# Performance work log

Measured on AMD Instinct MI355X. Metric: run time of the kernel, lower is better.

The kernel has to match this reference:

```python
import jax, jax.numpy as jnp
import numpy as np

B, T, K, V = 64, 256, 32, 32  # batch, trace_len, net_k, vocab_len


def setup_inputs() -> dict:
    key = jax.random.key(0)
    k1, k2, k3 = jax.random.split(key, 3)
    x = jax.random.uniform(k1, (B, T, V), dtype=jnp.float32)
    w_right = jax.random.normal(k2, (K, K + 1), dtype=jnp.float32)
    w_op = jax.random.normal(k3, (K, 5 + V), dtype=jnp.float32)
    return {"x": x, "w_right": w_right, "w_op": w_op}


def _myrelu(z):
    # CenteredLayer: x<0 -> 0.01*x ; x>1 -> 0.01*x + 0.99 ; else identity
    return jnp.where(z < 0, 0.01 * z, jnp.where(z > 1, 0.01 * z + 0.99, z))


def reference(x, w_right, w_op):
    Bs, Ts, Vs = x.shape
    Ks = w_right.shape[0]
    # cal_softmax()
    sm_op = jax.nn.softmax(w_op, axis=1)
    op_w = sm_op[:, :5].T          # (5, K) operator selection weights
    atom_w = sm_op[:, 5:].T        # (V, K)
    right_w = jax.nn.softmax(w_right, axis=1)[:, :-1].T  # (K, K)

    # atom_x is loop-invariant (x and atom_w do not change across iterations)
    atom_x = jnp.einsum('btv,vk->btk', x, atom_w)  # (B, T, K)
    zcol = jnp.zeros((Bs, Ts, 1), x.dtype)   # last_x (always zeros)
    zrow = jnp.zeros((Bs, 1, Ks), x.dtype)   # end_x  (always zeros)

    def step(all_x, _):
        left = jnp.concatenate([all_x[:, :, 1:], zcol], axis=2)          # shift node dim
        right = jnp.einsum('btk,kj->btj', all_x, right_w)                # right-child mix
        nxt = all_x[:, 1:]                                               # (B, T-1, K)
        X_left = jnp.concatenate(
            [jnp.concatenate([nxt[:, :, 1:], zcol[:, 1:]], axis=2), zrow], axis=1)
        nxt_full = jnp.concatenate([nxt, zrow], axis=1)                  # (B, T, K)
        until = right + _myrelu(left + nxt_full - 1.0)
        new = _myrelu(atom_x
                      + (1.0 - left) * op_w[1]            # not
                      + X_left * op_w[3]                  # next (X)
                      + (left + right - 1.0) * op_w[2]    # and
                      + until * op_w[4])                  # until
        return new, None

    init = jnp.zeros((Bs, Ts, Ks), x.dtype)
    all_x, _ = jax.lax.scan(step, init, None, length=Ts + Ks)
    return jax.nn.sigmoid((all_x - 0.5) * 5.0)
```

## Files before the change

### kernel.cpp

```cpp
#include <hip/hip_runtime.h>
#include <math.h>

#define BB 64
#define TT 256
#define KK 32
#define VV 32
#define CH 64
#define PH 32
#define ROWS (CH + PH)
#define NPHASE ((TT + KK) / PH)
#define BPB (TT / CH)
#define NW (ROWS / 16)

#define RW_OFF    0
#define WOP_OFF   1024
#define ATOM_OFF  2240
#define STATE_OFF (ATOM_OFF + BB*TT*KK)

typedef __attribute__((ext_vector_type(8))) short short8;
typedef __attribute__((ext_vector_type(4))) float floatx4;

__device__ __forceinline__ float myrelu(float z) {
    float c = fminf(fmaxf(z, 0.f), 1.f);
    return fmaf(0.01f, z, 0.99f * c);
}
__device__ __forceinline__ ushort f2bf(float f) {
    union { float f; unsigned int u; } v; v.f = f;
    unsigned int r = v.u + 0x7fffu + ((v.u >> 16) & 1u);
    return (ushort)(r >> 16);
}

__global__ void prep_kernel(const float* __restrict__ w_right,
                            const float* __restrict__ w_op,
                            float* __restrict__ ws) {
    int tid = threadIdx.x;
    float* rw  = ws + RW_OFF;
    float* wop = ws + WOP_OFF;
    if (tid < KK) {
        float v[37];
        float m = -1e30f;
        #pragma unroll
        for (int i = 0; i < 37; ++i) { v[i] = w_op[tid * 37 + i]; m = fmaxf(m, v[i]); }
        float s = 0.f;
        #pragma unroll
        for (int i = 0; i < 37; ++i) { v[i] = expf(v[i] - m); s += v[i]; }
        float inv = 1.f / s;
        #pragma unroll
        for (int i = 0; i < 37; ++i) wop[i * KK + tid] = v[i] * inv;
    } else if (tid < 2 * KK) {
        int r = tid - KK;
        float v[KK + 1];
        float m = -1e30f;
        #pragma unroll
        for (int i = 0; i <= KK; ++i) { v[i] = w_right[r * (KK + 1) + i]; m = fmaxf(m, v[i]); }
        float s = 0.f;
        #pragma unroll
        for (int i = 0; i <= KK; ++i) { v[i] = expf(v[i] - m); s += v[i]; }
        float inv = 1.f / s;
        #pragma unroll
        for (int c = 0; c < KK; ++c) rw[c * KK + r] = v[c] * inv;
    }
}

__global__ void atomx_kernel(const float* __restrict__ x, float* __restrict__ ws) {
    const float* aw = ws + WOP_OFF + 5 * KK;
    float* atom = ws + ATOM_OFF;
    int tid = threadIdx.x;
    int k  = tid & (KK - 1);
    int bt = blockIdx.x * 8 + (tid >> 5);
    const float* xrow = x + bt * VV;
    float acc = 0.f;
    #pragma unroll
    for (int v = 0; v < VV; ++v) acc = fmaf(xrow[v], aw[v * KK + k], acc);
    atom[bt * KK + k] = acc;
}

__global__ __launch_bounds__(384, 1)
void phase_kernel(float* __restrict__ ws, float* __restrict__ out,
                  int first, int last) {
    __shared__ float brow[2][NW + 1][36];

    const float* rw   = ws + RW_OFF;
    const float* wop  = ws + WOP_OFF;
    const float* atom = ws + ATOM_OFF;
    float*      state = ws + STATE_OFF;

    int tid  = threadIdx.x;
    int lane = tid & 63;
    int rt   = tid >> 6;
    int lr   = lane & 15;
    int hi   = lane >> 4;
    int b  = blockIdx.x / BPB;
    int c  = blockIdx.x % BPB;
    int lo = c * CH;
    int t0 = lo + rt * 16 + lr;
    bool active = (lo + rt * 16) < TT;

    for (int i = tid; i < 2 * (NW + 1) * 36; i += 384)
        (&brow[0][0][0])[i] = 0.f;

    float* gs = state + (size_t)b * TT * KK;

    float y[8];
    #pragma unroll
    for (int q = 0; q < 8; ++q) y[q] = 0.f;
    if (active && !first) {
        float4 v0 = *reinterpret_cast<const float4*>(&gs[t0 * KK + hi * 8]);
        float4 v1 = *reinterpret_cast<const float4*>(&gs[t0 * KK + hi * 8 + 4]);
        y[0] = v0.x; y[1] = v0.y; y[2] = v0.z; y[3] = v0.w;
        y[4] = v1.x; y[5] = v1.y; y[6] = v1.z; y[7] = v1.w;
    }

    float c0[8], d1[8], w2v[8], w3v[8], w4v[8];
    {
        float4 av0 = make_float4(0, 0, 0, 0), av1 = make_float4(0, 0, 0, 0);
        if (active) {
            av0 = *reinterpret_cast<const float4*>(&atom[((size_t)b * TT + t0) * KK + hi * 8]);
            av1 = *reinterpret_cast<const float4*>(&atom[((size_t)b * TT + t0) * KK + hi * 8 + 4]);
        }
        float av[8] = {av0.x, av0.y, av0.z, av0.w, av1.x, av1.y, av1.z, av1.w};
        #pragma unroll
        for (int q = 0; q < 8; ++q) {
            int j = hi * 8 + q;
            float w1 = wop[1 * KK + j];
            float w2 = wop[2 * KK + j];
            c0[q]  = av[q] + w1 - w2;
            d1[q]  = w2 - w1;
            w2v[q] = w2;
            w3v[q] = wop[3 * KK + j];
            w4v[q] = wop[4 * KK + j];
        }
    }

    short8 af0, af1;
    {
        int col0 = ((lr >> 2) << 3) | (lr & 3);
        #pragma unroll
        for (int q = 0; q < 8; ++q) {
            af0[q] = (short)f2bf(rw[(hi * 8 + q) * KK + col0]);
            af1[q] = (short)f2bf(rw[(hi * 8 + q) * KK + col0 + 4]);
        }
    }

    __syncthreads();
    if (active && lr == 0) {
        *reinterpret_cast<float4*>(&brow[0][rt][hi * 8])     = make_float4(y[0], y[1], y[2], y[3]);
        *reinterpret_cast<float4*>(&brow[0][rt][hi * 8 + 4]) = make_float4(y[4], y[5], y[6], y[7]);
    }
    __syncthreads();

    for (int s = 0; s < PH; ++s) {
        int cur = s & 1;
        if (active) {
            unsigned bw0, bw1, bw2, bw3;
            asm("v_cvt_pk_bf16_f32 %0, %1, %2" : "=v"(bw0) : "v"(y[0]), "v"(y[1]));
            asm("v_cvt_pk_bf16_f32 %0, %1, %2" : "=v"(bw1) : "v"(y[2]), "v"(y[3]));
            asm("v_cvt_pk_bf16_f32 %0, %1, %2" : "=v"(bw2) : "v"(y[4]), "v"(y[5]));
            asm("v_cvt_pk_bf16_f32 %0, %1, %2" : "=v"(bw3) : "v"(y[6]), "v"(y[7]));
            union { unsigned u[4]; short8 v; } bu;
            bu.u[0] = bw0; bu.u[1] = bw1; bu.u[2] = bw2; bu.u[3] = bw3;
            floatx4 acc0 = __builtin_amdgcn_mfma_f32_16x16x32_bf16(
                af0, bu.v, (floatx4){0.f, 0.f, 0.f, 0.f}, 0, 0, 0);
            floatx4 acc1 = __builtin_amdgcn_mfma_f32_16x16x32_bf16(
                af1, bu.v, (floatx4){0.f, 0.f, 0.f, 0.f}, 0, 0, 0);

            float nx[8];
            #pragma unroll
            for (int q = 0; q < 8; ++q) nx[q] = __shfl(y[q], lane + 1, 64);
            float lb = __shfl(y[0], lane + 16, 64);
            float xb = __shfl(y[0], lane + 17, 64);
            if (lr == 15) {
                float4 n0 = *reinterpret_cast<const float4*>(&brow[cur][rt + 1][hi * 8]);
                float4 n1 = *reinterpret_cast<const float4*>(&brow[cur][rt + 1][hi * 8 + 4]);
                nx[0] = n0.x; nx[1] = n0.y; nx[2] = n0.z; nx[3] = n0.w;
                nx[4] = n1.x; nx[5] = n1.y; nx[6] = n1.z; nx[7] = n1.w;
                xb = brow[cur][rt + 1][hi * 8 + 8];
            } else if (hi == 3) {
                xb = 0.f;
            }
            if (hi == 3) lb = 0.f;

            float le[8], xl[8];
            #pragma unroll
            for (int q = 0; q < 7; ++q) { le[q] = y[q + 1]; xl[q] = nx[q + 1]; }
            le[7] = lb; xl[7] = xb;

            #pragma unroll
            for (int q = 0; q < 8; ++q) {
                float rtv = (q < 4) ? acc0[q] : acc1[q - 4];
                float a = le[q] + nx[q] - 1.f;
                float until = rtv + myrelu(a);
                float z = fmaf(until, w4v[q],
                          fmaf(xl[q], w3v[q],
                          fmaf(rtv, w2v[q],
                          fmaf(le[q], d1[q], c0[q]))));
                y[q] = myrelu(z);
            }
        }
        if (active && lr == 0) {
            *reinterpret_cast<float4*>(&brow[cur ^ 1][rt][hi * 8])     = make_float4(y[0], y[1], y[2], y[3]);
            *reinterpret_cast<float4*>(&brow[cur ^ 1][rt][hi * 8 + 4]) = make_float4(y[4], y[5], y[6], y[7]);
        }
        __syncthreads();
    }

    if (rt < CH / 16) {
        if (last) {
            float* op = out + ((size_t)b * TT + t0) * KK + hi * 8;
            float o[8];
            #pragma unroll
            for (int q = 0; q < 8; ++q)
                o[q] = 1.f / (1.f + __expf(-5.f * (y[q] - 0.5f)));
            *reinterpret_cast<float4*>(&op[0]) = make_float4(o[0], o[1], o[2], o[3]);
            *reinterpret_cast<float4*>(&op[4]) = make_float4(o[4], o[5], o[6], o[7]);
        } else {
            *reinterpret_cast<float4*>(&gs[t0 * KK + hi * 8])     = make_float4(y[0], y[1], y[2], y[3]);
            *reinterpret_cast<float4*>(&gs[t0 * KK + hi * 8 + 4]) = make_float4(y[4], y[5], y[6], y[7]);
        }
    }
}

extern "C" void kernel_launch(void* const* d_in, const int* in_sizes, int n_in,
                              void* d_out, int out_size, void* d_ws, size_t ws_size,
                              hipStream_t stream) {
    const float* x       = (const float*)d_in[0];
    const float* w_right = (const float*)d_in[1];
    const float* w_op    = (const float*)d_in[2];
    float* ws  = (float*)d_ws;
    float* out = (float*)d_out;

    prep_kernel<<<1, 64, 0, stream>>>(w_right, w_op, ws);
    atomx_kernel<<<BB * TT / 8, 256, 0, stream>>>(x, ws);
    for (int p = 0; p < NPHASE; ++p)
        phase_kernel<<<BB * BPB, 384, 0, stream>>>(ws, out, p == 0, p == NPHASE - 1);
}
```

Baseline: 201.7 us.

## Fuse phase launches into one cooperative persistent kernel with flag-based neighbor sync

Replaces the nine separate phase kernel launches with a single cooperative kernel that loops over phases. Adjacent chunk blocks exchange halo rows through global memory, guarded by per-block release/acquire flags. The per-step math is also reworked: the atom/op constants go into the MFMA accumulator init, the right-mix weights are pre-scaled by w2+w4, and the until-relu is rewritten with fmed3. Neighbor shuffles now use DPP and bpermute. This removes launch overhead and global round trips between phases, at the cost of spin-wait synchronization and requiring all 256 blocks to be co-resident.

```diff
diff --git a/kernel.cpp b/kernel.cpp
--- a/kernel.cpp
+++ b/kernel.cpp
@@ -16,18 +16,22 @@
 #define WOP_OFF   1024
 #define ATOM_OFF  2240
 #define STATE_OFF (ATOM_OFF + BB*TT*KK)
+#define FLAG_OFF  (STATE_OFF + BB*TT*KK)
 
 typedef __attribute__((ext_vector_type(8))) short short8;
 typedef __attribute__((ext_vector_type(4))) float floatx4;
 
 __device__ __forceinline__ float myrelu(float z) {
-    float c = fminf(fmaxf(z, 0.f), 1.f);
-    return fmaf(0.01f, z, 0.99f * c);
+    return fmaf(0.01f, z, 0.99f * __builtin_amdgcn_fmed3f(z, 0.f, 1.f));
 }
 __device__ __forceinline__ ushort f2bf(float f) {
     union { float f; unsigned int u; } v; v.f = f;
     unsigned int r = v.u + 0x7fffu + ((v.u >> 16) & 1u);
     return (ushort)(r >> 16);
+}
+__device__ __forceinline__ float dpp_shl1(float v) {
+    return __int_as_float(__builtin_amdgcn_update_dpp(
+        0, __float_as_int(v), 0x101 , 0xF, 0xF, true));
 }
 
 __global__ void prep_kernel(const float* __restrict__ w_right,
@@ -66,6 +70,7 @@
     const float* aw = ws + WOP_OFF + 5 * KK;
     float* atom = ws + ATOM_OFF;
     int tid = threadIdx.x;
+    if (blockIdx.x == 0 && tid < BB * BPB) ((int*)(ws + FLAG_OFF))[tid] = 0;
     int k  = tid & (KK - 1);
     int bt = blockIdx.x * 8 + (tid >> 5);
     const float* xrow = x + bt * VV;
@@ -76,14 +81,14 @@
 }
 
 __global__ __launch_bounds__(384, 1)
-void phase_kernel(float* __restrict__ ws, float* __restrict__ out,
-                  int first, int last) {
+void phase_all_kernel(float* __restrict__ ws, float* __restrict__ out) {
     __shared__ float brow[2][NW + 1][36];
 
     const float* rw   = ws + RW_OFF;
     const float* wop  = ws + WOP_OFF;
     const float* atom = ws + ATOM_OFF;
     float*      state = ws + STATE_OFF;
+    int*        flags = (int*)(ws + FLAG_OFF);
 
     int tid  = threadIdx.x;
     int lane = tid & 63;
@@ -104,119 +109,149 @@
     float y[8];
     #pragma unroll
     for (int q = 0; q < 8; ++q) y[q] = 0.f;
-    if (active && !first) {
-        float4 v0 = *reinterpret_cast<const float4*>(&gs[t0 * KK + hi * 8]);
-        float4 v1 = *reinterpret_cast<const float4*>(&gs[t0 * KK + hi * 8 + 4]);
-        y[0] = v0.x; y[1] = v0.y; y[2] = v0.z; y[3] = v0.w;
-        y[4] = v1.x; y[5] = v1.y; y[6] = v1.z; y[7] = v1.w;
-    }
-
-    float c0[8], d1[8], w2v[8], w3v[8], w4v[8];
+
+    float c0p[8], d1p[8], w3v[8], w4n[8], w4c[8];
     {
-        float4 av0 = make_float4(0, 0, 0, 0), av1 = make_float4(0, 0, 0, 0);
+        float av[8] = {0, 0, 0, 0, 0, 0, 0, 0};
         if (active) {
-            av0 = *reinterpret_cast<const float4*>(&atom[((size_t)b * TT + t0) * KK + hi * 8]);
-            av1 = *reinterpret_cast<const float4*>(&atom[((size_t)b * TT + t0) * KK + hi * 8 + 4]);
-        }
-        float av[8] = {av0.x, av0.y, av0.z, av0.w, av1.x, av1.y, av1.z, av1.w};
+            float4 a0 = *reinterpret_cast<const float4*>(&atom[((size_t)b * TT + t0) * KK + hi * 8]);
+            float4 a1 = *reinterpret_cast<const float4*>(&atom[((size_t)b * TT + t0) * KK + hi * 8 + 4]);
+            av[0] = a0.x; av[1] = a0.y; av[2] = a0.z; av[3] = a0.w;
+            av[4] = a1.x; av[5] = a1.y; av[6] = a1.z; av[7] = a1.w;
+        }
         #pragma unroll
         for (int q = 0; q < 8; ++q) {
             int j = hi * 8 + q;
             float w1 = wop[1 * KK + j];
             float w2 = wop[2 * KK + j];
-            c0[q]  = av[q] + w1 - w2;
-            d1[q]  = w2 - w1;
-            w2v[q] = w2;
-            w3v[q] = wop[3 * KK + j];
-            w4v[q] = wop[4 * KK + j];
+            float w3 = wop[3 * KK + j];
+            float w4 = wop[4 * KK + j];
+            c0p[q] = av[q] + w1 - w2 - w4;
+            d1p[q] = (w2 - w1) + 0.01f * w4;
+            w4n[q] = 0.01f * w4;
+            w4c[q] = 0.99f * w4;
+            w3v[q] = w3;
         }
     }
 
     short8 af0, af1;
     {
         int col0 = ((lr >> 2) << 3) | (lr & 3);
+        float s0 = wop[2 * KK + col0]     + wop[4 * KK + col0];
+        float s1 = wop[2 * KK + col0 + 4] + wop[4 * KK + col0 + 4];
         #pragma unroll
         for (int q = 0; q < 8; ++q) {
-            af0[q] = (short)f2bf(rw[(hi * 8 + q) * KK + col0]);
-            af1[q] = (short)f2bf(rw[(hi * 8 + q) * KK + col0 + 4]);
-        }
-    }
-
+            af0[q] = (short)f2bf(rw[(hi * 8 + q) * KK + col0] * s0);
+            af1[q] = (short)f2bf(rw[(hi * 8 + q) * KK + col0 + 4] * s1);
+        }
+    }
+
+    int pidx = ((lane + 16) & 63) << 2;
     __syncthreads();
-    if (active && lr == 0) {
-        *reinterpret_cast<float4*>(&brow[0][rt][hi * 8])     = make_float4(y[0], y[1], y[2], y[3]);
-        *reinterpret_cast<float4*>(&brow[0][rt][hi * 8 + 4]) = make_float4(y[4], y[5], y[6], y[7]);
-    }
-    __syncthreads();
-
-    for (int s = 0; s < PH; ++s) {
-        int cur = s & 1;
-        if (active) {
-            unsigned bw0, bw1, bw2, bw3;
-            asm("v_cvt_pk_bf16_f32 %0, %1, %2" : "=v"(bw0) : "v"(y[0]), "v"(y[1]));
-            asm("v_cvt_pk_bf16_f32 %0, %1, %2" : "=v"(bw1) : "v"(y[2]), "v"(y[3]));
-            asm("v_cvt_pk_bf16_f32 %0, %1, %2" : "=v"(bw2) : "v"(y[4]), "v"(y[5]));
-            asm("v_cvt_pk_bf16_f32 %0, %1, %2" : "=v"(bw3) : "v"(y[6]), "v"(y[7]));
-            union { unsigned u[4]; short8 v; } bu;
-            bu.u[0] = bw0; bu.u[1] = bw1; bu.u[2] = bw2; bu.u[3] = bw3;
-            floatx4 acc0 = __builtin_amdgcn_mfma_f32_16x16x32_bf16(
-                af0, bu.v, (floatx4){0.f, 0.f, 0.f, 0.f}, 0, 0, 0);
-            floatx4 acc1 = __builtin_amdgcn_mfma_f32_16x16x32_bf16(
-                af1, bu.v, (floatx4){0.f, 0.f, 0.f, 0.f}, 0, 0, 0);
-
-            float nx[8];
-            #pragma unroll
-            for (int q = 0; q < 8; ++q) nx[q] = __shfl(y[q], lane + 1, 64);
-            float lb = __shfl(y[0], lane + 16, 64);
-            float xb = __shfl(y[0], lane + 17, 64);
-            if (lr == 15) {
-                float4 n0 = *reinterpret_cast<const float4*>(&brow[cur][rt + 1][hi * 8]);
-                float4 n1 = *reinterpret_cast<const float4*>(&brow[cur][rt + 1][hi * 8 + 4]);
-                nx[0] = n0.x; nx[1] = n0.y; nx[2] = n0.z; nx[3] = n0.w;
-                nx[4] = n1.x; nx[5] = n1.y; nx[6] = n1.z; nx[7] = n1.w;
-                xb = brow[cur][rt + 1][hi * 8 + 8];
-            } else if (hi == 3) {
-                xb = 0.f;
+
+    for (int p = 0; p < NPHASE; ++p) {
+        for (int s = 0; s < PH; ++s) {
+            int cur = s & 1;
+            if (active) {
+                unsigned bw0, bw1, bw2, bw3;
+                asm("v_cvt_pk_bf16_f32 %0, %1, %2" : "=v"(bw0) : "v"(y[0]), "v"(y[1]));
+                asm("v_cvt_pk_bf16_f32 %0, %1, %2" : "=v"(bw1) : "v"(y[2]), "v"(y[3]));
+                asm("v_cvt_pk_bf16_f32 %0, %1, %2" : "=v"(bw2) : "v"(y[4]), "v"(y[5]));
+                asm("v_cvt_pk_bf16_f32 %0, %1, %2" : "=v"(bw3) : "v"(y[6]), "v"(y[7]));
+                union { unsigned u[4]; short8 v; } bu;
+                bu.u[0] = bw0; bu.u[1] = bw1; bu.u[2] = bw2; bu.u[3] = bw3;
+                floatx4 acc0 = __builtin_amdgcn_mfma_f32_16x16x32_bf16(
+                    af0, bu.v, (floatx4){c0p[0], c0p[1], c0p[2], c0p[3]}, 0, 0, 0);
+                floatx4 acc1 = __builtin_amdgcn_mfma_f32_16x16x32_bf16(
+                    af1, bu.v, (floatx4){c0p[4], c0p[5], c0p[6], c0p[7]}, 0, 0, 0);
+
+                float nx[8];
+                #pragma unroll
+                for (int q = 0; q < 8; ++q) nx[q] = dpp_shl1(y[q]);
+                float lbr = __int_as_float(__builtin_amdgcn_ds_bpermute(pidx, __float_as_int(y[0])));
+                float lb  = (hi == 3) ? 0.f : lbr;
+                float xb  = dpp_shl1(lb);
+                if (hi == 3) xb = 0.f;
+                if (lr == 15) {
+                    float4 n0 = *reinterpret_cast<const float4*>(&brow[cur][rt + 1][hi * 8]);
+                    float4 n1 = *reinterpret_cast<const float4*>(&brow[cur][rt + 1][hi * 8 + 4]);
+                    nx[0] = n0.x; nx[1] = n0.y; nx[2] = n0.z; nx[3] = n0.w;
+                    nx[4] = n1.x; nx[5] = n1.y; nx[6] = n1.z; nx[7] = n1.w;
+                    xb = brow[cur][rt + 1][hi * 8 + 8];
+                }
+
+                float le[8], xl[8];
+                #pragma unroll
+                for (int q = 0; q < 7; ++q) { le[q] = y[q + 1]; xl[q] = nx[q + 1]; }
+                le[7] = lb; xl[7] = xb;
+
+                #pragma unroll
+                for (int q = 0; q < 8; ++q) {
+                    float accq = (q < 4) ? acc0[q] : acc1[q - 4];
+                    float sm = le[q] + nx[q];
+                    float t  = __builtin_amdgcn_fmed3f(sm, 1.f, 2.f);
+                    float z  = fmaf(le[q], d1p[q],
+                               fmaf(nx[q], w4n[q],
+                               fmaf(t, w4c[q],
+                               fmaf(xl[q], w3v[q], accq))));
+                    y[q] = myrelu(z);
+                }
+                if (lr == 0) {
+                    *reinterpret_cast<float4*>(&brow[cur ^ 1][rt][hi * 8])     = make_float4(y[0], y[1], y[2], y[3]);
+                    *reinterpret_cast<float4*>(&brow[cur ^ 1][rt][hi * 8 + 4]) = make_float4(y[4], y[5], y[6], y[7]);
+                }
             }
-            if (hi == 3) lb = 0.f;
-
-            float le[8], xl[8];
-            #pragma unroll
-            for (int q = 0; q < 7; ++q) { le[q] = y[q + 1]; xl[q] = nx[q + 1]; }
-            le[7] = lb; xl[7] = xb;
-
-            #pragma unroll
-            for (int q = 0; q < 8; ++q) {
-                float rtv = (q < 4) ? acc0[q] : acc1[q - 4];
-                float a = le[q] + nx[q] - 1.f;
-                float until = rtv + myrelu(a);
-                float z = fmaf(until, w4v[q],
-                          fmaf(xl[q], w3v[q],
-                          fmaf(rtv, w2v[q],
-                          fmaf(le[q], d1[q], c0[q]))));
-                y[q] = myrelu(z);
+            __syncthreads();
+        }
+        if (p == NPHASE - 1) break;
+
+        if (rt < 2 && c > 0) {
+            unsigned long long* gp =
+                reinterpret_cast<unsigned long long*>(gs + (size_t)t0 * KK + hi * 8);
+            union { float f[8]; unsigned long long u[4]; } pk;
+            #pragma unroll
+            for (int q = 0; q < 8; ++q) pk.f[q] = y[q];
+            #pragma unroll
+            for (int w = 0; w < 4; ++w)
+                __hip_atomic_store(&gp[w], pk.u[w], __ATOMIC_RELAXED, __HIP_MEMORY_SCOPE_AGENT);
+        }
+        __syncthreads();
+        if (tid == 0) {
+            if (c > 0)
+                __hip_atomic_store(&flags[b * BPB + c], p + 1,
+                                   __ATOMIC_RELEASE, __HIP_MEMORY_SCOPE_AGENT);
+            if (c < BPB - 1) {
+                while (__hip_atomic_load(&flags[b * BPB + c + 1],
+                                         __ATOMIC_ACQUIRE, __HIP_MEMORY_SCOPE_AGENT) < p + 1)
+                    __builtin_amdgcn_s_sleep(2);
             }
         }
-        if (active && lr == 0) {
-            *reinterpret_cast<float4*>(&brow[cur ^ 1][rt][hi * 8])     = make_float4(y[0], y[1], y[2], y[3]);
-            *reinterpret_cast<float4*>(&brow[cur ^ 1][rt][hi * 8 + 4]) = make_float4(y[4], y[5], y[6], y[7]);
-        }
         __syncthreads();
+        if (active && rt >= CH / 16) {
+            unsigned long long* gp =
+                reinterpret_cast<unsigned long long*>(gs + (size_t)t0 * KK + hi * 8);
+            union { float f[8]; unsigned long long u[4]; } pk;
+            #pragma unroll
+            for (int w = 0; w < 4; ++w)
+                pk.u[w] = __hip_atomic_load(&gp[w], __ATOMIC_RELAXED, __HIP_MEMORY_SCOPE_AGENT);
+            #pragma unroll
+            for (int q = 0; q < 8; ++q) y[q] = pk.f[q];
+            if (lr == 0) {
+                *reinterpret_cast<float4*>(&brow[0][rt][hi * 8])     = make_float4(y[0], y[1], y[2], y[3]);
+                *reinterpret_cast<float4*>(&brow[0][rt][hi * 8 + 4]) = make_float4(y[4], y[5], y[6], y[7]);
+            }
+        }
+        __syncthreads();
     }
 
     if (rt < CH / 16) {
-        if (last) {
-            float* op = out + ((size_t)b * TT + t0) * KK + hi * 8;
-            float o[8];
-            #pragma unroll
-            for (int q = 0; q < 8; ++q)
-                o[q] = 1.f / (1.f + __expf(-5.f * (y[q] - 0.5f)));
-            *reinterpret_cast<float4*>(&op[0]) = make_float4(o[0], o[1], o[2], o[3]);
-            *reinterpret_cast<float4*>(&op[4]) = make_float4(o[4], o[5], o[6], o[7]);
-        } else {
-            *reinterpret_cast<float4*>(&gs[t0 * KK + hi * 8])     = make_float4(y[0], y[1], y[2], y[3]);
-            *reinterpret_cast<float4*>(&gs[t0 * KK + hi * 8 + 4]) = make_float4(y[4], y[5], y[6], y[7]);
-        }
+        float* op = out + ((size_t)b * TT + t0) * KK + hi * 8;
+        float o[8];
+        #pragma unroll
+        for (int q = 0; q < 8; ++q)
+            o[q] = 1.f / (1.f + __expf(-5.f * (y[q] - 0.5f)));
+        *reinterpret_cast<float4*>(&op[0]) = make_float4(o[0], o[1], o[2], o[3]);
+        *reinterpret_cast<float4*>(&op[4]) = make_float4(o[4], o[5], o[6], o[7]);
     }
 }
 
@@ -231,6 +266,8 @@
 
     prep_kernel<<<1, 64, 0, stream>>>(w_right, w_op, ws);
     atomx_kernel<<<BB * TT / 8, 256, 0, stream>>>(x, ws);
-    for (int p = 0; p < NPHASE; ++p)
-        phase_kernel<<<BB * BPB, 384, 0, stream>>>(ws, out, p == 0, p == NPHASE - 1);
-}
+
+    void* args[] = { (void*)&ws, (void*)&out };
+    hipLaunchCooperativeKernel((void*)phase_all_kernel,
+                               dim3(BB * BPB), dim3(384), args, 0, stream);
+}
```

Result: faster. 184.7 us (-8.4%).
